# Kernel tuning notes

Hardware: AMD Instinct MI355X
Metric: run time of the kernel (lower is better)

The kernel has to match this reference:

```python
import jax, jax.numpy as jnp
import numpy as np

BSZ, L, D_Q, S_Q = 2, 2048, 512, 4
EPS = 1e-6


def quat_mul(a, b):
    ar, ai, aj, ak = a[..., 0], a[..., 1], a[..., 2], a[..., 3]
    br, bi, bj, bk = b[..., 0], b[..., 1], b[..., 2], b[..., 3]
    return jnp.stack((
        ar * br - ai * bi - aj * bj - ak * bk,
        ar * bi + ai * br + aj * bk - ak * bj,
        ar * bj - ai * bk + aj * br + ak * bi,
        ar * bk + ai * bj - aj * bi + ak * br,
    ), axis=-1)


def quat_inv(q):
    r, i, j, k = q[..., 0], q[..., 1], q[..., 2], q[..., 3]
    s = 1.0 / (r * r + i * i + j * j + k * k + EPS)
    return jnp.stack((r * s, -i * s, -j * s, -k * s), axis=-1)


def setup_inputs() -> dict:
    key = jax.random.key(0)
    ks = jax.random.split(key, 8)
    u = jax.random.normal(ks[0], (BSZ, L, D_Q, 4), dtype=jnp.float32)
    dt = jax.random.uniform(ks[1], (BSZ, L, D_Q), dtype=jnp.float32)
    B_in = jax.random.normal(ks[2], (BSZ, L, S_Q, 4), dtype=jnp.float32)
    C_in = jax.random.normal(ks[3], (BSZ, L, S_Q, 4), dtype=jnp.float32)
    # A_log init: log(arange(1, S_q+1)) repeated over D_q rows
    A_log = jnp.tile(jnp.log(jnp.arange(1, S_Q + 1, dtype=jnp.float32)), (D_Q, 1))
    A_i = jax.random.normal(ks[4], (D_Q, S_Q), dtype=jnp.float32) * 0.01
    A_j = jax.random.normal(ks[5], (D_Q, S_Q), dtype=jnp.float32) * 0.01
    A_k = jax.random.normal(ks[6], (D_Q, S_Q), dtype=jnp.float32) * 0.01
    return {"u": u, "dt": dt, "B_in": B_in, "C_in": C_in,
            "A_log": A_log, "A_i": A_i, "A_j": A_j, "A_k": A_k}


def reference(u, dt, B_in, C_in, A_log, A_i, A_j, A_k):
    # A quaternion: real part -exp(A_log), imaginary parts A_i/j/k  [D_q, S_q, 4]
    A_quat = jnp.stack([-jnp.exp(A_log), A_i, A_j, A_k], axis=-1)
    dt_b = dt[..., None, None]                      # [B, L, D_q, 1, 1]
    z = dt_b * A_quat                               # [B, L, D_q, S_q, 4]
    one = jnp.zeros_like(z).at[..., 0].set(1.0)     # quaternion identity
    num = one + 0.5 * z
    den = one - 0.5 * z
    den_inv = quat_inv(den)
    q = quat_mul(den_inv, num)                      # Cayley transition [B,L,D_q,S_q,4]
    dB = quat_mul(den_inv * dt_b, B_in[:, :, None])  # [B,L,D_q,S_q,4]
    Bu = quat_mul(dB, u[:, :, :, None])             # [B,L,D_q,S_q,4]

    def step(h, qb):
        qt, but = qb
        h = quat_mul(qt, h) + but
        return h, h

    h0 = jnp.zeros((u.shape[0], u.shape[2], A_quat.shape[1], 4), u.dtype)
    _, h_all = jax.lax.scan(step, h0, (jnp.swapaxes(q, 0, 1), jnp.swapaxes(Bu, 0, 1)))
    h_all = jnp.swapaxes(h_all, 0, 1)               # [B, L, D_q, S_q, 4]
    yh = quat_mul(C_in[:, :, None], h_all)
    return yh.sum(axis=3)                           # [B, L, D_q, 4]
```

## Files before the change

### kernel.cpp

```cpp
#include <hip/hip_runtime.h>

#define BSZ   2
#define LSEQ  2048
#define DQ    512
#define SQ    4
#define EPSQ  1e-6f

typedef float nfloat4 __attribute__((ext_vector_type(4)));
typedef float nfloat2 __attribute__((ext_vector_type(2)));

__device__ __forceinline__ nfloat2 mk2(float x, float y) { nfloat2 v; v.x = x; v.y = y; return v; }

struct PQuat { nfloat2 ri, jk; };

__device__ __forceinline__ PQuat pq_of(const float4 v) {
    PQuat p; p.ri = mk2(v.x, v.y); p.jk = mk2(v.z, v.w); return p;
}
__device__ __forceinline__ float4 f4_of(const PQuat p) {
    return make_float4(p.ri.x, p.ri.y, p.jk.x, p.jk.y);
}

__device__ __forceinline__ PQuat pqmul(const PQuat a, const PQuat b) {
    const float ar = a.ri.x, ai = a.ri.y, aj = a.jk.x, ak = a.jk.y;
    PQuat o;
    o.ri = ar*b.ri + ai*mk2(-b.ri.y,  b.ri.x)
         + aj*mk2(-b.jk.x,  b.jk.y) + ak*mk2(-b.jk.y, -b.jk.x);
    o.jk = ar*b.jk + ai*mk2(-b.jk.y,  b.jk.x)
         + aj*mk2( b.ri.x, -b.ri.y) + ak*mk2( b.ri.y,  b.ri.x);
    return o;
}

__device__ __forceinline__ PQuat pqmuladd(const PQuat a, const PQuat b, const PQuat c) {
    const float ar = a.ri.x, ai = a.ri.y, aj = a.jk.x, ak = a.jk.y;
    PQuat o;
    o.ri = c.ri + ar*b.ri + ai*mk2(-b.ri.y,  b.ri.x)
         + aj*mk2(-b.jk.x,  b.jk.y) + ak*mk2(-b.jk.y, -b.jk.x);
    o.jk = c.jk + ar*b.jk + ai*mk2(-b.jk.y,  b.jk.x)
         + aj*mk2( b.ri.x, -b.ri.y) + ak*mk2( b.ri.y,  b.ri.x);
    return o;
}

__device__ __forceinline__ void cayley_pk(const float a, const PQuat hA,
                                          const PQuat B, const PQuat U,
                                          PQuat& q, PQuat& Bu) {
    const nfloat2 w_ri = a * hA.ri;
    const nfloat2 w_jk = a * hA.jk;
    const float wr = w_ri.x, wi = w_ri.y;
    const float m  = wi*wi + w_jk.x*w_jk.x + w_jk.y*w_jk.y;
    const float e  = 1.0f - wr;
    const float dd = e*e + m + EPSQ;
    const float sv = __builtin_amdgcn_rcpf(dd);
    const float s2 = sv + sv;
    q.ri = mk2(sv * (1.0f - (wr*wr + m)), s2 * wi);
    q.jk = s2 * w_jk;
    PQuat cd; cd.ri = mk2(e, wi); cd.jk = w_jk;
    const PQuat cb = pqmul(cd, B);
    const float as = a * sv;
    PQuat dB; dB.ri = as * cb.ri; dB.jk = as * cb.jk;
    Bu = pqmul(dB, U);
}

__device__ __forceinline__ PQuat load_hA_pk(const float* __restrict__ Alog,
                                            const float* __restrict__ Ai,
                                            const float* __restrict__ Aj,
                                            const float* __restrict__ Ak, int idx) {
    PQuat p;
    p.ri = mk2(-0.5f * __expf(Alog[idx]), 0.5f * Ai[idx]);
    p.jk = mk2( 0.5f * Aj[idx],           0.5f * Ak[idx]);
    return p;
}

struct Quat { float r, i, j, k; };
__device__ __forceinline__ Quat qmul(const Quat a, const Quat b) {
    Quat o;
    o.r = a.r*b.r - a.i*b.i - a.j*b.j - a.k*b.k;
    o.i = a.r*b.i + a.i*b.r + a.j*b.k - a.k*b.j;
    o.j = a.r*b.j - a.i*b.k + a.j*b.r + a.k*b.i;
    o.k = a.r*b.k + a.i*b.j - a.j*b.i + a.k*b.r;
    return o;
}
__device__ __forceinline__ Quat qmuladd(const Quat a, const Quat b, const Quat c) {
    Quat o;
    o.r = c.r + a.r*b.r - a.i*b.i - a.j*b.j - a.k*b.k;
    o.i = c.i + a.r*b.i + a.i*b.r + a.j*b.k - a.k*b.j;
    o.j = c.j + a.r*b.j - a.i*b.k + a.j*b.r + a.k*b.i;
    o.k = c.k + a.r*b.k + a.i*b.j - a.j*b.i + a.k*b.r;
    return o;
}
__device__ __forceinline__ Quat q_of(const float4 v) { return Quat{v.x, v.y, v.z, v.w}; }
__device__ __forceinline__ float4 f4s_of(const Quat q) { return make_float4(q.r, q.i, q.j, q.k); }

template<int NCH>
__global__ __launch_bounds__(256, 6) void qssm_pass1(
    const float* __restrict__ u, const float* __restrict__ dt,
    const float* __restrict__ Bin,
    const float* __restrict__ Alog, const float* __restrict__ Ai,
    const float* __restrict__ Aj,   const float* __restrict__ Ak,
    float4* __restrict__ WQ, float4* __restrict__ WB)
{
    constexpr int CH = LSEQ / NCH;
    const int d  = blockIdx.x * 256 + threadIdx.x;
    const int c  = blockIdx.y;
    const int b  = blockIdx.z >> 1;
    const int s0 = (blockIdx.z & 1) * 2;
    const int t0 = c * CH;

    PQuat hA[2];
    hA[0] = load_hA_pk(Alog, Ai, Aj, Ak, d*SQ + s0);
    hA[1] = load_hA_pk(Alog, Ai, Aj, Ak, d*SQ + s0 + 1);

    const int base = (b*LSEQ + t0);
    const float*  dtp = dt + (size_t)base*DQ + d;
    const float4* up  = (const float4*)u   + (size_t)base*DQ + d;
    const float4* Bp  = (const float4*)Bin + (size_t)base*SQ + s0;

    PQuat Q[2], Bc[2];
    {
        const float a  = *dtp;
        const PQuat U  = pq_of(*up);
#pragma unroll
        for (int ss = 0; ss < 2; ++ss) {
            PQuat q, Bu;
            cayley_pk(a, hA[ss], pq_of(Bp[ss]), U, q, Bu);
            Q[ss] = q; Bc[ss] = Bu;
        }
        dtp += DQ; up += DQ; Bp += SQ;
    }
#pragma unroll 2
    for (int j = 1; j < CH; ++j) {
        const float a  = *dtp;
        const PQuat U  = pq_of(*up);
#pragma unroll
        for (int ss = 0; ss < 2; ++ss) {
            PQuat q, Bu;
            cayley_pk(a, hA[ss], pq_of(Bp[ss]), U, q, Bu);
            Bc[ss] = pqmuladd(q, Bc[ss], Bu);
            Q[ss]  = pqmul(q, Q[ss]);
        }
        dtp += DQ; up += DQ; Bp += SQ;
    }
#pragma unroll
    for (int ss = 0; ss < 2; ++ss) {
        const size_t idx = ((size_t)(b*SQ + s0 + ss)*NCH + c)*DQ + d;
        WQ[idx] = f4_of(Q[ss]);
        WB[idx] = f4_of(Bc[ss]);
    }
}

template<int NCH>
__global__ __launch_bounds__(256) void qssm_pass2(
    const float4* __restrict__ WQ, float4* __restrict__ WB)
{
    constexpr int GS = 16;
    constexpr int NG = NCH / GS;
    __shared__ float4 QL[NG][16];
    __shared__ float4 BL[NG][16];
    __shared__ float4 HS[NG][16];

    const int t  = threadIdx.x;
    const int i  = t & 15;
    const int g  = t >> 4;
    const int bs = blockIdx.x >> 5;
    const int d  = (blockIdx.x & 31) * 16 + i;
    const size_t chbase = (size_t)bs * NCH * DQ + d;

    size_t idx = chbase + (size_t)(g * GS) * DQ;
    Quat Qa = q_of(WQ[idx]);
    Quat Ba = q_of(WB[idx]);
#pragma unroll
    for (int j = 1; j < GS; ++j) {
        idx += DQ;
        const Quat Qc = q_of(WQ[idx]);
        const Quat Bc = q_of(WB[idx]);
        Ba = qmuladd(Qc, Ba, Bc);
        Qa = qmul(Qc, Qa);
    }
    QL[g][i] = f4s_of(Qa);
    BL[g][i] = f4s_of(Ba);
    __syncthreads();

    if (t < 16) {
        Quat h{0.f, 0.f, 0.f, 0.f};
#pragma unroll
        for (int gg = 0; gg < NG; ++gg) {
            HS[gg][t] = f4s_of(h);
            h = qmuladd(q_of(QL[gg][t]), h, q_of(BL[gg][t]));
        }
    }
    __syncthreads();

    Quat h = q_of(HS[g][i]);
    idx = chbase + (size_t)(g * GS) * DQ;
#pragma unroll
    for (int j = 0; j < GS; ++j) {
        const Quat Qc = q_of(WQ[idx]);
        const Quat Bc = q_of(WB[idx]);
        WB[idx] = f4s_of(h);
        h = qmuladd(Qc, h, Bc);
        idx += DQ;
    }
}

template<int NCH>
__global__ __launch_bounds__(256, 6) void qssm_pass3(
    const float* __restrict__ u, const float* __restrict__ dt,
    const float* __restrict__ Bin, const float* __restrict__ Cin,
    const float* __restrict__ Alog, const float* __restrict__ Ai,
    const float* __restrict__ Aj,   const float* __restrict__ Ak,
    const float4* __restrict__ WB, float* __restrict__ out)
{
    constexpr int CH = LSEQ / NCH;
    const int t    = threadIdx.x;
    const int lane = t & 63;
    const int wv   = t >> 6;
    const int dl   = lane & 31;
    const int sh   = lane >> 5;
    const int s0   = sh * 2;
    const int d = blockIdx.x * 128 + wv * 32 + dl;
    const int c = blockIdx.y;
    const int b = blockIdx.z;
    const int t0 = c * CH;

    PQuat hA[2];
    PQuat h[2];
#pragma unroll
    for (int ss = 0; ss < 2; ++ss) {
        hA[ss] = load_hA_pk(Alog, Ai, Aj, Ak, d*SQ + s0 + ss);
        h[ss] = pq_of(WB[((size_t)(b*SQ + s0 + ss)*NCH + c)*DQ + d]);
    }
    const int base = (b*LSEQ + t0);
    const float*  dtp  = dt + (size_t)base*DQ + d;
    const float4* up   = (const float4*)u   + (size_t)base*DQ + d;
    const float4* Bp   = (const float4*)Bin + (size_t)base*SQ + s0;
    const float4* Cp   = (const float4*)Cin + (size_t)base*SQ + s0;
    nfloat4*      outp = (nfloat4*)out + (size_t)base*DQ + d;

#pragma unroll 2
    for (int j = 0; j < CH; ++j) {
        const float a  = *dtp;
        const PQuat U  = pq_of(*up);
        PQuat y; y.ri = mk2(0.f, 0.f); y.jk = mk2(0.f, 0.f);
#pragma unroll
        for (int ss = 0; ss < 2; ++ss) {
            const PQuat Cq = pq_of(Cp[ss]);
            PQuat q, Bu;
            cayley_pk(a, hA[ss], pq_of(Bp[ss]), U, q, Bu);
            h[ss] = pqmuladd(q, h[ss], Bu);
            y = pqmuladd(Cq, h[ss], y);
        }
        float yr = y.ri.x + __shfl_xor(y.ri.x, 32);
        float yi = y.ri.y + __shfl_xor(y.ri.y, 32);
        float yj = y.jk.x + __shfl_xor(y.jk.x, 32);
        float yk = y.jk.y + __shfl_xor(y.jk.y, 32);
        if (sh == 0) {
            const nfloat4 yv = {yr, yi, yj, yk};
            __builtin_nontemporal_store(yv, outp);
        }
        dtp += DQ; up += DQ; Bp += SQ; Cp += SQ; outp += DQ;
    }
}

template<int NCH>
static void launch_all(const float* u, const float* dt, const float* Bin,
                       const float* Cin, const float* Alog, const float* Ai,
                       const float* Aj, const float* Ak,
                       float* out, void* d_ws, hipStream_t stream) {
    const size_t elems = (size_t)BSZ * SQ * NCH * DQ;
    float4* WQ = (float4*)d_ws;
    float4* WB = WQ + elems;
    dim3 g1(DQ / 256, NCH, BSZ * 2);
    qssm_pass1<NCH><<<g1, 256, 0, stream>>>(u, dt, Bin, Alog, Ai, Aj, Ak, WQ, WB);
    qssm_pass2<NCH><<<(BSZ*SQ*DQ)/16, 16*(NCH/16), 0, stream>>>(WQ, WB);
    dim3 g3(DQ / 128, NCH, BSZ);
    qssm_pass3<NCH><<<g3, 256, 0, stream>>>(u, dt, Bin, Cin, Alog, Ai, Aj, Ak, WB, out);
}

extern "C" void kernel_launch(void* const* d_in, const int* in_sizes, int n_in,
                              void* d_out, int out_size, void* d_ws, size_t ws_size,
                              hipStream_t stream) {
    const float* u    = (const float*)d_in[0];
    const float* dt   = (const float*)d_in[1];
    const float* Bin  = (const float*)d_in[2];
    const float* Cin  = (const float*)d_in[3];
    const float* Alog = (const float*)d_in[4];
    const float* Ai   = (const float*)d_in[5];
    const float* Aj   = (const float*)d_in[6];
    const float* Ak   = (const float*)d_in[7];
    float* out = (float*)d_out;

    auto ws_need = [](int nch) -> size_t {
        return 2ull * BSZ * SQ * (size_t)nch * DQ * sizeof(float4);
    };
    if (ws_size >= ws_need(256)) {
        launch_all<256>(u, dt, Bin, Cin, Alog, Ai, Aj, Ak, out, d_ws, stream);
    } else if (ws_size >= ws_need(128)) {
        launch_all<128>(u, dt, Bin, Cin, Alog, Ai, Aj, Ak, out, d_ws, stream);
    } else {
        launch_all<64>(u, dt, Bin, Cin, Alog, Ai, Aj, Ak, out, d_ws, stream);
    }
}
```

Measured before the change: 151.4 us.

## Precompute Cayley constants, remap pass1 thread layout, shrink pass2 group size

Precomputes |A/2|^2 and -2*Re(A/2) per state so the Cayley denominator and real numerator come from a couple of FMAs on dt and dt^2 instead of forming w explicitly. Pass1 now puts both state halves in one block (128 d per block, threads split across s), so u and dt loads are shared within a block rather than split across blocks. Pass2 halves the serial group size and doubles threads per block, giving a shorter sequential chain and more parallelism. This trades some register use and a different rounding order for fewer ALU ops and shorter serial scans.

```diff
diff --git a/kernel.cpp b/kernel.cpp
--- a/kernel.cpp
+++ b/kernel.cpp
@@ -40,34 +40,37 @@
     return o;
 }
 
-__device__ __forceinline__ void cayley_pk(const float a, const PQuat hA,
+struct HA { float r, i; nfloat2 jk; float p2, n2r; };
+
+__device__ __forceinline__ HA load_hA(const float* __restrict__ Alog,
+                                      const float* __restrict__ Ai,
+                                      const float* __restrict__ Aj,
+                                      const float* __restrict__ Ak, int idx) {
+    HA h;
+    h.r  = -0.5f * __expf(Alog[idx]);
+    h.i  =  0.5f * Ai[idx];
+    h.jk = mk2(0.5f * Aj[idx], 0.5f * Ak[idx]);
+    h.p2 = h.r*h.r + h.i*h.i + h.jk.x*h.jk.x + h.jk.y*h.jk.y;
+    h.n2r = -2.0f * h.r;
+    return h;
+}
+
+__device__ __forceinline__ void cayley_pk(const float a, const float aa, const HA& hA,
                                           const PQuat B, const PQuat U,
                                           PQuat& q, PQuat& Bu) {
-    const nfloat2 w_ri = a * hA.ri;
-    const nfloat2 w_jk = a * hA.jk;
-    const float wr = w_ri.x, wi = w_ri.y;
-    const float m  = wi*wi + w_jk.x*w_jk.x + w_jk.y*w_jk.y;
-    const float e  = 1.0f - wr;
-    const float dd = e*e + m + EPSQ;
+    const float dd = __builtin_fmaf(aa, hA.p2, __builtin_fmaf(a, hA.n2r, 1.0f + EPSQ));
     const float sv = __builtin_amdgcn_rcpf(dd);
-    const float s2 = sv + sv;
-    q.ri = mk2(sv * (1.0f - (wr*wr + m)), s2 * wi);
-    q.jk = s2 * w_jk;
-    PQuat cd; cd.ri = mk2(e, wi); cd.jk = w_jk;
+    const float nr = __builtin_fmaf(-aa, hA.p2, 1.0f);
+    const float as = a * sv;
+    const float s2a = as + as;
+    q.ri = mk2(nr * sv, s2a * hA.i);
+    q.jk = s2a * hA.jk;
+    PQuat cd;
+    cd.ri = mk2(__builtin_fmaf(-a, hA.r, 1.0f), a * hA.i);
+    cd.jk = a * hA.jk;
     const PQuat cb = pqmul(cd, B);
-    const float as = a * sv;
     PQuat dB; dB.ri = as * cb.ri; dB.jk = as * cb.jk;
     Bu = pqmul(dB, U);
-}
-
-__device__ __forceinline__ PQuat load_hA_pk(const float* __restrict__ Alog,
-                                            const float* __restrict__ Ai,
-                                            const float* __restrict__ Aj,
-                                            const float* __restrict__ Ak, int idx) {
-    PQuat p;
-    p.ri = mk2(-0.5f * __expf(Alog[idx]), 0.5f * Ai[idx]);
-    p.jk = mk2( 0.5f * Aj[idx],           0.5f * Ak[idx]);
-    return p;
 }
 
 struct Quat { float r, i, j, k; };
@@ -99,15 +102,18 @@
     float4* __restrict__ WQ, float4* __restrict__ WB)
 {
     constexpr int CH = LSEQ / NCH;
-    const int d  = blockIdx.x * 256 + threadIdx.x;
+    const int t  = threadIdx.x;
+    const int dl = t & 127;
+    const int sh = t >> 7;
+    const int d  = blockIdx.x * 128 + dl;
     const int c  = blockIdx.y;
-    const int b  = blockIdx.z >> 1;
-    const int s0 = (blockIdx.z & 1) * 2;
+    const int b  = blockIdx.z;
+    const int s0 = sh * 2;
     const int t0 = c * CH;
 
-    PQuat hA[2];
-    hA[0] = load_hA_pk(Alog, Ai, Aj, Ak, d*SQ + s0);
-    hA[1] = load_hA_pk(Alog, Ai, Aj, Ak, d*SQ + s0 + 1);
+    HA hA[2];
+    hA[0] = load_hA(Alog, Ai, Aj, Ak, d*SQ + s0);
+    hA[1] = load_hA(Alog, Ai, Aj, Ak, d*SQ + s0 + 1);
 
     const int base = (b*LSEQ + t0);
     const float*  dtp = dt + (size_t)base*DQ + d;
@@ -117,11 +123,12 @@
     PQuat Q[2], Bc[2];
     {
         const float a  = *dtp;
+        const float aa = a * a;
         const PQuat U  = pq_of(*up);
 #pragma unroll
         for (int ss = 0; ss < 2; ++ss) {
             PQuat q, Bu;
-            cayley_pk(a, hA[ss], pq_of(Bp[ss]), U, q, Bu);
+            cayley_pk(a, aa, hA[ss], pq_of(Bp[ss]), U, q, Bu);
             Q[ss] = q; Bc[ss] = Bu;
         }
         dtp += DQ; up += DQ; Bp += SQ;
@@ -129,11 +136,12 @@
 #pragma unroll 2
     for (int j = 1; j < CH; ++j) {
         const float a  = *dtp;
+        const float aa = a * a;
         const PQuat U  = pq_of(*up);
 #pragma unroll
         for (int ss = 0; ss < 2; ++ss) {
             PQuat q, Bu;
-            cayley_pk(a, hA[ss], pq_of(Bp[ss]), U, q, Bu);
+            cayley_pk(a, aa, hA[ss], pq_of(Bp[ss]), U, q, Bu);
             Bc[ss] = pqmuladd(q, Bc[ss], Bu);
             Q[ss]  = pqmul(q, Q[ss]);
         }
@@ -148,10 +156,10 @@
 }
 
 template<int NCH>
-__global__ __launch_bounds__(256) void qssm_pass2(
+__global__ __launch_bounds__(512) void qssm_pass2(
     const float4* __restrict__ WQ, float4* __restrict__ WB)
 {
-    constexpr int GS = 16;
+    constexpr int GS = 8;
     constexpr int NG = NCH / GS;
     __shared__ float4 QL[NG][16];
     __shared__ float4 BL[NG][16];
@@ -221,11 +229,11 @@
     const int b = blockIdx.z;
     const int t0 = c * CH;
 
-    PQuat hA[2];
+    HA hA[2];
     PQuat h[2];
 #pragma unroll
     for (int ss = 0; ss < 2; ++ss) {
-        hA[ss] = load_hA_pk(Alog, Ai, Aj, Ak, d*SQ + s0 + ss);
+        hA[ss] = load_hA(Alog, Ai, Aj, Ak, d*SQ + s0 + ss);
         h[ss] = pq_of(WB[((size_t)(b*SQ + s0 + ss)*NCH + c)*DQ + d]);
     }
     const int base = (b*LSEQ + t0);
@@ -238,13 +246,14 @@
 #pragma unroll 2
     for (int j = 0; j < CH; ++j) {
         const float a  = *dtp;
+        const float aa = a * a;
         const PQuat U  = pq_of(*up);
         PQuat y; y.ri = mk2(0.f, 0.f); y.jk = mk2(0.f, 0.f);
 #pragma unroll
         for (int ss = 0; ss < 2; ++ss) {
             const PQuat Cq = pq_of(Cp[ss]);
             PQuat q, Bu;
-            cayley_pk(a, hA[ss], pq_of(Bp[ss]), U, q, Bu);
+            cayley_pk(a, aa, hA[ss], pq_of(Bp[ss]), U, q, Bu);
             h[ss] = pqmuladd(q, h[ss], Bu);
             y = pqmuladd(Cq, h[ss], y);
         }
@@ -268,9 +277,9 @@
     const size_t elems = (size_t)BSZ * SQ * NCH * DQ;
     float4* WQ = (float4*)d_ws;
     float4* WB = WQ + elems;
-    dim3 g1(DQ / 256, NCH, BSZ * 2);
+    dim3 g1(DQ / 128, NCH, BSZ);
     qssm_pass1<NCH><<<g1, 256, 0, stream>>>(u, dt, Bin, Alog, Ai, Aj, Ak, WQ, WB);
-    qssm_pass2<NCH><<<(BSZ*SQ*DQ)/16, 16*(NCH/16), 0, stream>>>(WQ, WB);
+    qssm_pass2<NCH><<<(BSZ*SQ*DQ)/16, 16*(NCH/8), 0, stream>>>(WQ, WB);
     dim3 g3(DQ / 128, NCH, BSZ);
     qssm_pass3<NCH><<<g3, 256, 0, stream>>>(u, dt, Bin, Cin, Alog, Ai, Aj, Ak, WB, out);
 }
```

After: 156.1 us. +3.1%, slower.
